# Kernel optimization log

Hardware: AMD Instinct MI355X
Metric: run time of the kernel (lower is better)

The kernel has to match this reference:

```python
import jax, jax.numpy as jnp
import numpy as np

N_NODES = 100000
N_EDGES = 600000
D_IN = 128
D_HID = 128
N_CLASSES = 64


def setup_inputs() -> dict:
    key = jax.random.key(0)
    ks = jax.random.split(key, 8)
    x = jax.random.normal(ks[0], (N_NODES, D_IN), dtype=jnp.float32)
    src = jax.random.randint(ks[1], (N_EDGES,), 0, N_NODES, dtype=jnp.int32)
    dst = jax.random.randint(ks[2], (N_EDGES,), 0, N_NODES, dtype=jnp.int32)
    s = 1.0 / np.sqrt(D_IN)
    W_self1 = jax.random.normal(ks[3], (D_IN, D_HID), dtype=jnp.float32) * s
    W_neigh1 = jax.random.normal(ks[4], (D_IN, D_HID), dtype=jnp.float32) * s
    b1 = jnp.zeros((D_HID,), dtype=jnp.float32)
    s2 = 1.0 / np.sqrt(D_HID)
    W_self2 = jax.random.normal(ks[5], (D_HID, N_CLASSES), dtype=jnp.float32) * s2
    W_neigh2 = jax.random.normal(ks[6], (D_HID, N_CLASSES), dtype=jnp.float32) * s2
    b2 = jnp.zeros((N_CLASSES,), dtype=jnp.float32)
    return {"x": x, "src": src, "dst": dst,
            "W_self1": W_self1, "W_neigh1": W_neigh1, "b1": b1,
            "W_self2": W_self2, "W_neigh2": W_neigh2, "b2": b2}


def _sage_conv(h, src, dst, W_self, W_neigh, b):
    # mean aggregation over in-neighbors (DGL SAGEConv 'mean')
    n = h.shape[0]
    nbr_sum = jax.ops.segment_sum(h[src], dst, num_segments=n)  # [N, d]
    deg = jax.ops.segment_sum(jnp.ones(src.shape, h.dtype), dst, num_segments=n)
    nbr_mean = nbr_sum / jnp.maximum(deg, 1.0)[:, None]
    return h @ W_self + nbr_mean @ W_neigh + b


def reference(x, src, dst, W_self1, W_neigh1, b1, W_self2, W_neigh2, b2):
    # dropout is identity in eval mode
    h = _sage_conv(x, src, dst, W_self1, W_neigh1, b1)
    h = jax.nn.relu(h)
    h = _sage_conv(h, src, dst, W_self2, W_neigh2, b2)
    return h
```

## Files before the change

kernel.cpp:

```cpp
#include <hip/hip_runtime.h>

#define N_NODES 100000
#define N_EDGES 600000
#define K_DIM 128
#define M2 64
#define NT_TILES ((N_NODES + 63) / 64)
#define GEMM_GRID 256

#define NBKT 800
#define NPB 125
#define HIST_BLOCKS 64
#define EPB (N_EDGES / HIST_BLOCKS)

using frag_ab = __attribute__((ext_vector_type(8))) short;
using frag_cd = __attribute__((ext_vector_type(4))) float;

__device__ __forceinline__ unsigned short f2b(float f) {
  unsigned u = __builtin_bit_cast(unsigned, f);
  u = (u + 0x7fffu + ((u >> 16) & 1u)) >> 16;
  return (unsigned short)u;
}

__device__ __forceinline__ void gload_lds16(const void* gsrc, void* ldst) {
  __builtin_amdgcn_global_load_lds(
      (const __attribute__((address_space(1))) void*)gsrc,
      (__attribute__((address_space(3))) void*)ldst, 16, 0, 0);
}

__device__ __forceinline__ void lgkm_barrier() {
  __builtin_amdgcn_sched_barrier(0);
  asm volatile("s_waitcnt lgkmcnt(0)" ::: "memory");
  __builtin_amdgcn_s_barrier();
  __builtin_amdgcn_sched_barrier(0);
}

#define XB_BLOCKS ((N_NODES * K_DIM / 4 + 255) / 256)
#define W_ELEMS ((128 + 128 + 64 + 64) * 128)
#define WB_BLOCKS ((W_ELEMS + 255) / 256)
__global__ __launch_bounds__(256) void conv_all(const float* __restrict__ x,
                                                unsigned short* __restrict__ xb,
                                                const float* __restrict__ Ws1,
                                                const float* __restrict__ Wn1,
                                                const float* __restrict__ Ws2,
                                                const float* __restrict__ Wn2,
                                                unsigned short* __restrict__ Ws1T,
                                                unsigned short* __restrict__ Wn1T,
                                                unsigned short* __restrict__ Ws2T,
                                                unsigned short* __restrict__ Wn2T,
                                                const int* __restrict__ dst,
                                                int* __restrict__ pos,
                                                int* __restrict__ gbucket,
                                                int* __restrict__ base_tbl) {
  __shared__ int lcnt[NBKT];
  if (blockIdx.x < HIST_BLOCKS) {
    int tid = threadIdx.x;
    for (int i = tid; i < NBKT; i += 256) lcnt[i] = 0;
    __syncthreads();
    int e0 = blockIdx.x * EPB;
    for (int e = e0 + tid; e < e0 + EPB; e += 256) {
      int b = dst[e] / NPB;
      pos[e] = atomicAdd(&lcnt[b], 1);
    }
    __syncthreads();
    for (int i = tid; i < NBKT; i += 256) {
      int c = lcnt[i];
      if (c) base_tbl[blockIdx.x * NBKT + i] = atomicAdd(&gbucket[i], c);
    }
  } else if (blockIdx.x < HIST_BLOCKS + XB_BLOCKS) {
    long i = (long)(blockIdx.x - HIST_BLOCKS) * 256 + threadIdx.x;
    if (i >= (long)N_NODES * K_DIM / 4) return;
    float4 v = *(const float4*)(x + i * 4);
    ushort4 o;
    o.x = f2b(v.x); o.y = f2b(v.y); o.z = f2b(v.z); o.w = f2b(v.w);
    *(ushort4*)(xb + i * 4) = o;
  } else {
    int i = (blockIdx.x - HIST_BLOCKS - XB_BLOCKS) * 256 + threadIdx.x;
    if (i >= W_ELEMS) return;
    const float* W;
    unsigned short* WT;
    int M, li;
    if (i < 128 * 128)               { W = Ws1; WT = Ws1T; M = 128; li = i; }
    else if (i < 2 * 128 * 128)      { W = Wn1; WT = Wn1T; M = 128; li = i - 128 * 128; }
    else if (i < 2 * 128 * 128 + 64 * 128) { W = Ws2; WT = Ws2T; M = 64; li = i - 2 * 128 * 128; }
    else                             { W = Wn2; WT = Wn2T; M = 64; li = i - 2 * 128 * 128 - 64 * 128; }
    int n = li >> 7, k = li & 127;
    WT[li] = f2b(W[k * M + n]);
  }
}

__global__ __launch_bounds__(1024) void scan_buckets(const int* __restrict__ gbucket,
                                                     int* __restrict__ bucket_start,
                                                     int* __restrict__ row_ptr) {
  __shared__ int s[1024];
  int tid = threadIdx.x;
  int v = (tid < NBKT) ? gbucket[tid] : 0;
  s[tid] = v;
  __syncthreads();
  for (int off = 1; off < 1024; off <<= 1) {
    int t = (tid >= off) ? s[tid - off] : 0;
    __syncthreads();
    s[tid] += t;
    __syncthreads();
  }
  if (tid < NBKT) bucket_start[tid] = s[tid] - v;
  if (tid == 0) { bucket_start[NBKT] = N_EDGES; row_ptr[N_NODES] = N_EDGES; }
}

__global__ __launch_bounds__(256) void bucket_scatter(const int* __restrict__ src,
                                                      const int* __restrict__ dst,
                                                      const int* __restrict__ pos,
                                                      const int* __restrict__ bucket_start,
                                                      const int* __restrict__ base_tbl,
                                                      int* __restrict__ ebuf_src,
                                                      int* __restrict__ ebuf_ln) {
  int e = blockIdx.x * 256 + threadIdx.x;
  if (e >= N_EDGES) return;
  int d = dst[e];
  int b = d / NPB;
  int p = bucket_start[b] + base_tbl[(e / EPB) * NBKT + b] + pos[e];
  ebuf_src[p] = src[e];
  ebuf_ln[p] = d - b * NPB;
}

__global__ __launch_bounds__(256) void bucket_csr(const int* __restrict__ ebuf_src,
                                                  const int* __restrict__ ebuf_ln,
                                                  const int* __restrict__ bucket_start,
                                                  int* __restrict__ row_ptr,
                                                  int* __restrict__ csr_src) {
  __shared__ int cnt[128];
  int tid = threadIdx.x, b = blockIdx.x;
  int bs = bucket_start[b], be = bucket_start[b + 1];
  for (int i = tid; i < 128; i += 256) cnt[i] = 0;
  __syncthreads();
  int ln[6], lp[6];
#pragma unroll
  for (int j = 0; j < 6; ++j) {
    int p = bs + tid + j * 256;
    if (p < be) { ln[j] = ebuf_ln[p]; lp[j] = atomicAdd(&cnt[ln[j]], 1); }
  }
  __syncthreads();
  for (int off = 1; off < 128; off <<= 1) {
    int t = 0;
    if (tid < 128 && tid >= off) t = cnt[tid - off];
    __syncthreads();
    if (tid < 128) cnt[tid] += t;
    __syncthreads();
  }
  for (int i = tid; i < NPB; i += 256)
    row_ptr[b * NPB + i] = bs + (i ? cnt[i - 1] : 0);
#pragma unroll
  for (int j = 0; j < 6; ++j) {
    int p = bs + tid + j * 256;
    if (p < be) {
      int l = ln[j];
      csr_src[bs + (l ? cnt[l - 1] : 0) + lp[j]] = ebuf_src[p];
    }
  }
}

__global__ __launch_bounds__(256) void aggregate128(const unsigned short* __restrict__ xb,
                                                    const int* __restrict__ row_ptr,
                                                    const int* __restrict__ csr_src,
                                                    unsigned short* __restrict__ agg, int n) {
  int t = blockIdx.x * blockDim.x + threadIdx.x;
  int node = t >> 4;
  int c = (t & 15) << 3;
  if (node >= n) return;
  int beg = row_ptr[node], end = row_ptr[node + 1];
  float acc[8];
#pragma unroll
  for (int j = 0; j < 8; ++j) acc[j] = 0.f;

  if (end > beg) {
    for (int e0 = beg; e0 < end; e0 += 8) {
      int idx[8];
#pragma unroll
      for (int p = 0; p < 8; ++p) idx[p] = csr_src[min(e0 + p, end - 1)];
      uint4 v[8];
#pragma unroll
      for (int p = 0; p < 8; ++p) v[p] = *(const uint4*)(xb + (size_t)idx[p] * K_DIM + c);
#pragma unroll
      for (int p = 0; p < 8; ++p) {
        float m = (e0 + p < end) ? 1.f : 0.f;
        unsigned u[4] = {v[p].x, v[p].y, v[p].z, v[p].w};
#pragma unroll
        for (int j = 0; j < 4; ++j) {
          acc[2 * j]     += m * __builtin_bit_cast(float, u[j] << 16);
          acc[2 * j + 1] += m * __builtin_bit_cast(float, u[j] & 0xffff0000u);
        }
      }
    }
  }
  float inv = 1.0f / (float)max(end - beg, 1);
  uint4 o;
  unsigned* op = (unsigned*)&o;
#pragma unroll
  for (int j = 0; j < 4; ++j) {
    unsigned lo = f2b(acc[2 * j] * inv);
    unsigned hi = f2b(acc[2 * j + 1] * inv);
    op[j] = lo | (hi << 16);
  }
  *(uint4*)(agg + (size_t)node * K_DIM + c) = o;
}

__global__ __launch_bounds__(256) void aggregate64_add(const unsigned short* __restrict__ g,
                                                       const int* __restrict__ row_ptr,
                                                       const int* __restrict__ csr_src,
                                                       float* __restrict__ out, int n) {
  int t = blockIdx.x * blockDim.x + threadIdx.x;
  int node = t >> 3;
  int c = (t & 7) << 3;
  if (node >= n) return;
  int beg = row_ptr[node], end = row_ptr[node + 1];
  float acc[8];
#pragma unroll
  for (int j = 0; j < 8; ++j) acc[j] = 0.f;

  if (end > beg) {
    for (int e0 = beg; e0 < end; e0 += 8) {
      int idx[8];
#pragma unroll
      for (int p = 0; p < 8; ++p) idx[p] = csr_src[min(e0 + p, end - 1)];
      uint4 v[8];
#pragma unroll
      for (int p = 0; p < 8; ++p) v[p] = *(const uint4*)(g + (size_t)idx[p] * M2 + c);
#pragma unroll
      for (int p = 0; p < 8; ++p) {
        float m = (e0 + p < end) ? 1.f : 0.f;
        unsigned u[4] = {v[p].x, v[p].y, v[p].z, v[p].w};
#pragma unroll
        for (int j = 0; j < 4; ++j) {
          acc[2 * j]     += m * __builtin_bit_cast(float, u[j] << 16);
          acc[2 * j + 1] += m * __builtin_bit_cast(float, u[j] & 0xffff0000u);
        }
      }
    }
  }
  float inv = 1.0f / (float)max(end - beg, 1);
  float* op = out + (size_t)node * M2 + c;
  float4 o0 = *(float4*)(op);
  float4 o1 = *(float4*)(op + 4);
  o0.x += acc[0] * inv; o0.y += acc[1] * inv; o0.z += acc[2] * inv; o0.w += acc[3] * inv;
  o1.x += acc[4] * inv; o1.y += acc[5] * inv; o1.z += acc[6] * inv; o1.w += acc[7] * inv;
  *(float4*)(op) = o0;
  *(float4*)(op + 4) = o1;
}

__device__ __forceinline__ void stage_tile(const unsigned short* xb, const unsigned short* aggb,
                                           int t, char* dstbase, int tid, int wave, int N) {
#pragma unroll
  for (int it = 0; it < 2; ++it) {
    int L = it * 8192 + tid * 16;
    int row = L >> 8;
    int srb = (L & 255) ^ ((row & 7) << 4);
    int node = t * 64 + row;
    if (node >= N) node = N - 1;
    char* d = dstbase + it * 8192 + wave * 1024;
    gload_lds16((const char*)xb + (size_t)node * 256 + srb, d);
    gload_lds16((const char*)aggb + (size_t)node * 256 + srb, d + 16384);
  }
}

__global__ __launch_bounds__(512, 2) void sage_fused_gemm(const unsigned short* __restrict__ xb,
                                                          const unsigned short* __restrict__ aggb,
                                                          const unsigned short* __restrict__ Ws1T,
                                                          const unsigned short* __restrict__ Wn1T,
                                                          const float* __restrict__ b1,
                                                          const unsigned short* __restrict__ Ws2T,
                                                          const unsigned short* __restrict__ Wn2T,
                                                          const float* __restrict__ b2,
                                                          float* __restrict__ out,
                                                          unsigned short* __restrict__ g, int N) {
  __shared__ char sL[163840];

  const int tid = threadIdx.x;
  const int wave = tid >> 6;
  const int lane = tid & 63;
  const int l15 = lane & 15;
  const int q = lane >> 4;
  const int nodeq = wave >> 1;
  const int fhalf = wave & 1;
  const int fbase = fhalf * 64;

#pragma unroll
  for (int it = 0; it < 4; ++it) {
    int L = it * 8192 + tid * 16;
    int row = L >> 8;
    int srb = (L & 255) ^ ((row & 7) << 4);
    char* d = sL + it * 8192 + wave * 1024;
    gload_lds16((const char*)Ws1T + row * 256 + srb, d);
    gload_lds16((const char*)Wn1T + row * 256 + srb, d + 32768);
  }
#pragma unroll
  for (int it = 0; it < 2; ++it) {
    int L = it * 8192 + tid * 16;
    int row = L >> 8;
    int srb = (L & 255) ^ ((row & 7) << 4);
    char* d = sL + 65536 + it * 8192 + wave * 1024;
    gload_lds16((const char*)Ws2T + row * 256 + srb, d);
    gload_lds16((const char*)Wn2T + row * 256 + srb, d + 16384);
  }
  int tt = blockIdx.x;
  if (tt < NT_TILES) stage_tile(xb, aggb, tt, sL + 98304, tid, wave, N);

  float4 bv1[4], bv2[4];
#pragma unroll
  for (int ft = 0; ft < 4; ++ft) {
    bv1[ft] = *(const float4*)(b1 + fbase + ft * 16 + q * 4);
    bv2[ft] = *(const float4*)(b2 + ft * 16 + q * 4);
  }

  int li = 0;
  for (; tt < NT_TILES; tt += GEMM_GRID, ++li) {
    char* cur = sL + 98304 + (li & 1) * 32768;
    char* nxt = sL + 98304 + ((li + 1) & 1) * 32768;

    __syncthreads();

    if (tt + GEMM_GRID < NT_TILES)
      stage_tile(xb, aggb, tt + GEMM_GRID, nxt, tid, wave, N);

    frag_cd acc[4];
#pragma unroll
    for (int ft = 0; ft < 4; ++ft) acc[ft] = (frag_cd)(0.f);

    const int xrow = nodeq * 16 + l15;
    const int xswz = (xrow & 7) << 4;
#pragma unroll
    for (int kb = 0; kb < 4; ++kb) {
      int base = kb * 64 + q * 16;
      frag_ab axk = *(const frag_ab*)(cur + xrow * 256 + (base ^ xswz));
      frag_ab agk = *(const frag_ab*)(cur + 16384 + xrow * 256 + (base ^ xswz));
      frag_ab fs[4], fn[4];
#pragma unroll
      for (int ft = 0; ft < 4; ++ft) {
        int wrow = fbase + ft * 16 + l15;
        int woff = base ^ ((wrow & 7) << 4);
        fs[ft] = *(const frag_ab*)(sL + wrow * 256 + woff);
        fn[ft] = *(const frag_ab*)(sL + 32768 + wrow * 256 + woff);
      }
#pragma unroll
      for (int ft = 0; ft < 4; ++ft) {
        acc[ft] = __builtin_amdgcn_mfma_f32_16x16x32_bf16(fs[ft], axk, acc[ft], 0, 0, 0);
        acc[ft] = __builtin_amdgcn_mfma_f32_16x16x32_bf16(fn[ft], agk, acc[ft], 0, 0, 0);
      }
    }

    lgkm_barrier();

#pragma unroll
    for (int ft = 0; ft < 4; ++ft) {
      int f0 = fbase + ft * 16 + q * 4;
      ushort4 o;
      o.x = f2b(fmaxf(acc[ft][0] + bv1[ft].x, 0.f));
      o.y = f2b(fmaxf(acc[ft][1] + bv1[ft].y, 0.f));
      o.z = f2b(fmaxf(acc[ft][2] + bv1[ft].z, 0.f));
      o.w = f2b(fmaxf(acc[ft][3] + bv1[ft].w, 0.f));
      *(ushort4*)(cur + xrow * 256 + ((f0 * 2) ^ xswz)) = o;
    }

    lgkm_barrier();

    const char* w2b = sL + 65536 + fhalf * 16384;
    frag_cd acc2[4];
#pragma unroll
    for (int ft = 0; ft < 4; ++ft) acc2[ft] = (frag_cd)(0.f);

#pragma unroll
    for (int kb = 0; kb < 4; ++kb) {
      int base = kb * 64 + q * 16;
      frag_ab ah = *(const frag_ab*)(cur + xrow * 256 + (base ^ xswz));
      frag_ab w2[4];
#pragma unroll
      for (int ft = 0; ft < 4; ++ft) {
        int wr = ft * 16 + l15;
        w2[ft] = *(const frag_ab*)(w2b + wr * 256 + (base ^ ((wr & 7) << 4)));
      }
#pragma unroll
      for (int ft = 0; ft < 4; ++ft)
        acc2[ft] = __builtin_amdgcn_mfma_f32_16x16x32_bf16(w2[ft], ah, acc2[ft], 0, 0, 0);
    }

    int node = tt * 64 + nodeq * 16 + l15;
    if (node < N) {
      if (fhalf == 0) {
#pragma unroll
        for (int ft = 0; ft < 4; ++ft) {
          int f0 = ft * 16 + q * 4;
          float4 o;
          o.x = acc2[ft][0] + bv2[ft].x;
          o.y = acc2[ft][1] + bv2[ft].y;
          o.z = acc2[ft][2] + bv2[ft].z;
          o.w = acc2[ft][3] + bv2[ft].w;
          *(float4*)(out + (size_t)node * M2 + f0) = o;
        }
      } else {
#pragma unroll
        for (int ft = 0; ft < 4; ++ft) {
          int f0 = ft * 16 + q * 4;
          ushort4 o;
          o.x = f2b(acc2[ft][0]);
          o.y = f2b(acc2[ft][1]);
          o.z = f2b(acc2[ft][2]);
          o.w = f2b(acc2[ft][3]);
          *(ushort4*)(g + (size_t)node * M2 + f0) = o;
        }
      }
    }
  }
}

extern "C" void kernel_launch(void* const* d_in, const int* in_sizes, int n_in,
                              void* d_out, int out_size, void* d_ws, size_t ws_size,
                              hipStream_t stream) {
  const float* x   = (const float*)d_in[0];
  const int*   src = (const int*)d_in[1];
  const int*   dst = (const int*)d_in[2];
  const float* Ws1 = (const float*)d_in[3];
  const float* Wn1 = (const float*)d_in[4];
  const float* b1  = (const float*)d_in[5];
  const float* Ws2 = (const float*)d_in[6];
  const float* Wn2 = (const float*)d_in[7];
  const float* b2  = (const float*)d_in[8];
  float* out = (float*)d_out;

  char* ws = (char*)d_ws;
  size_t off = 0;
  auto alloc = [&](size_t bytes) {
    void* p = ws + off;
    off = (off + bytes + 4095) & ~(size_t)4095;
    return p;
  };
  int* row_ptr      = (int*)alloc((size_t)(N_NODES + 1) * 4);
  int* pos          = (int*)alloc((size_t)N_EDGES * 4);
  int* gbucket      = (int*)alloc((size_t)NBKT * 4);
  int* bucket_start = (int*)alloc((size_t)(NBKT + 1) * 4);
  int* base_tbl     = (int*)alloc((size_t)HIST_BLOCKS * NBKT * 4);
  int* ebuf_src     = (int*)alloc((size_t)N_EDGES * 4);
  int* ebuf_ln      = (int*)alloc((size_t)N_EDGES * 4);
  int* csr_src      = (int*)alloc((size_t)N_EDGES * 4);
  unsigned short* xb   = (unsigned short*)alloc((size_t)N_NODES * K_DIM * 2);
  unsigned short* aggb = (unsigned short*)alloc((size_t)N_NODES * K_DIM * 2);
  unsigned short* g    = (unsigned short*)alloc((size_t)N_NODES * M2 * 2);
  unsigned short* Ws1T = (unsigned short*)alloc((size_t)128 * 128 * 2);
  unsigned short* Wn1T = (unsigned short*)alloc((size_t)128 * 128 * 2);
  unsigned short* Ws2T = (unsigned short*)alloc((size_t)64 * 128 * 2);
  unsigned short* Wn2T = (unsigned short*)alloc((size_t)64 * 128 * 2);

  hipMemsetAsync(gbucket, 0, (size_t)NBKT * 4, stream);

  conv_all<<<HIST_BLOCKS + XB_BLOCKS + WB_BLOCKS, 256, 0, stream>>>(
      x, xb, Ws1, Wn1, Ws2, Wn2, Ws1T, Wn1T, Ws2T, Wn2T, dst, pos, gbucket, base_tbl);

  scan_buckets<<<1, 1024, 0, stream>>>(gbucket, bucket_start, row_ptr);
  bucket_scatter<<<(N_EDGES + 255) / 256, 256, 0, stream>>>(
      src, dst, pos, bucket_start, base_tbl, ebuf_src, ebuf_ln);
  bucket_csr<<<NBKT, 256, 0, stream>>>(ebuf_src, ebuf_ln, bucket_start, row_ptr, csr_src);

  {
    long t = (long)N_NODES * 16;
    aggregate128<<<(int)((t + 255) / 256), 256, 0, stream>>>(xb, row_ptr, csr_src, aggb, N_NODES);
  }

  sage_fused_gemm<<<GEMM_GRID, 512, 0, stream>>>(
      xb, aggb, Ws1T, Wn1T, b1, Ws2T, Wn2T, b2, out, g, N_NODES);

  {
    long t = (long)N_NODES * 8;
    aggregate64_add<<<(int)((t + 255) / 256), 256, 0, stream>>>(g, row_ptr, csr_src, out, N_NODES);
  }
}
```

Before: 211.9 us.

## Fuse bucket CSR build with layer-1 neighbor aggregation in one kernel

Merges the per-bucket CSR construction and the layer-1 mean aggregation into one kernel with 512 threads per bucket. Sorted source indices are kept in shared memory and reused directly for the gather, so csr_src and row_ptr are not re-read from global memory. This also removes one kernel launch. The cost is that aggregation now runs on only 800 blocks, which may lower parallelism and latency hiding. Each thread handles at most 3 edges, so a bucket with more than 1536 edges would silently drop edges; the shared buffer has the same 1536 capacity.

```diff
diff --git a/kernel.cpp b/kernel.cpp
--- a/kernel.cpp
+++ b/kernel.cpp
@@ -11,6 +11,7 @@
 #define NPB 125
 #define HIST_BLOCKS 64
 #define EPB (N_EDGES / HIST_BLOCKS)
+#define BKT_CAP 1536
 
 using frag_ab = __attribute__((ext_vector_type(8))) short;
 using frag_cd = __attribute__((ext_vector_type(4))) float;
@@ -122,21 +123,29 @@
   ebuf_ln[p] = d - b * NPB;
 }
 
-__global__ __launch_bounds__(256) void bucket_csr(const int* __restrict__ ebuf_src,
-                                                  const int* __restrict__ ebuf_ln,
-                                                  const int* __restrict__ bucket_start,
-                                                  int* __restrict__ row_ptr,
-                                                  int* __restrict__ csr_src) {
+__global__ __launch_bounds__(512) void bucket_csr_agg1(const unsigned short* __restrict__ xb,
+                                                       const int* __restrict__ ebuf_src,
+                                                       const int* __restrict__ ebuf_ln,
+                                                       const int* __restrict__ bucket_start,
+                                                       int* __restrict__ row_ptr,
+                                                       int* __restrict__ csr_src,
+                                                       unsigned short* __restrict__ aggb) {
   __shared__ int cnt[128];
+  __shared__ int sedge[BKT_CAP];
   int tid = threadIdx.x, b = blockIdx.x;
   int bs = bucket_start[b], be = bucket_start[b + 1];
-  for (int i = tid; i < 128; i += 256) cnt[i] = 0;
+  for (int i = tid; i < 128; i += 512) cnt[i] = 0;
   __syncthreads();
-  int ln[6], lp[6];
-#pragma unroll
-  for (int j = 0; j < 6; ++j) {
-    int p = bs + tid + j * 256;
-    if (p < be) { ln[j] = ebuf_ln[p]; lp[j] = atomicAdd(&cnt[ln[j]], 1); }
+
+  int ln[3], lp[3], sv[3];
+#pragma unroll
+  for (int j = 0; j < 3; ++j) {
+    int p = bs + tid + j * 512;
+    if (p < be) {
+      ln[j] = ebuf_ln[p];
+      sv[j] = ebuf_src[p];
+      lp[j] = atomicAdd(&cnt[ln[j]], 1);
+    }
   }
   __syncthreads();
   for (int off = 1; off < 128; off <<= 1) {
@@ -146,61 +155,60 @@
     if (tid < 128) cnt[tid] += t;
     __syncthreads();
   }
-  for (int i = tid; i < NPB; i += 256)
+  for (int i = tid; i < NPB; i += 512)
     row_ptr[b * NPB + i] = bs + (i ? cnt[i - 1] : 0);
 #pragma unroll
-  for (int j = 0; j < 6; ++j) {
-    int p = bs + tid + j * 256;
+  for (int j = 0; j < 3; ++j) {
+    int p = bs + tid + j * 512;
     if (p < be) {
       int l = ln[j];
-      csr_src[bs + (l ? cnt[l - 1] : 0) + lp[j]] = ebuf_src[p];
-    }
-  }
-}
-
-__global__ __launch_bounds__(256) void aggregate128(const unsigned short* __restrict__ xb,
-                                                    const int* __restrict__ row_ptr,
-                                                    const int* __restrict__ csr_src,
-                                                    unsigned short* __restrict__ agg, int n) {
-  int t = blockIdx.x * blockDim.x + threadIdx.x;
-  int node = t >> 4;
-  int c = (t & 15) << 3;
-  if (node >= n) return;
-  int beg = row_ptr[node], end = row_ptr[node + 1];
-  float acc[8];
-#pragma unroll
-  for (int j = 0; j < 8; ++j) acc[j] = 0.f;
-
-  if (end > beg) {
-    for (int e0 = beg; e0 < end; e0 += 8) {
-      int idx[8];
-#pragma unroll
-      for (int p = 0; p < 8; ++p) idx[p] = csr_src[min(e0 + p, end - 1)];
-      uint4 v[8];
-#pragma unroll
-      for (int p = 0; p < 8; ++p) v[p] = *(const uint4*)(xb + (size_t)idx[p] * K_DIM + c);
-#pragma unroll
-      for (int p = 0; p < 8; ++p) {
-        float m = (e0 + p < end) ? 1.f : 0.f;
-        unsigned u[4] = {v[p].x, v[p].y, v[p].z, v[p].w};
-#pragma unroll
-        for (int j = 0; j < 4; ++j) {
-          acc[2 * j]     += m * __builtin_bit_cast(float, u[j] << 16);
-          acc[2 * j + 1] += m * __builtin_bit_cast(float, u[j] & 0xffff0000u);
+      int loc = (l ? cnt[l - 1] : 0) + lp[j];
+      sedge[loc] = sv[j];
+      csr_src[bs + loc] = sv[j];
+    }
+  }
+  __syncthreads();
+
+  int nl = tid >> 4;
+  int c = (tid & 15) << 3;
+  for (int n0 = 0; n0 < NPB; n0 += 32) {
+    int node = n0 + nl;
+    if (node < NPB) {
+      int beg = node ? cnt[node - 1] : 0;
+      int end = cnt[node];
+      float acc[8];
+#pragma unroll
+      for (int j = 0; j < 8; ++j) acc[j] = 0.f;
+      for (int e0 = beg; e0 < end; e0 += 8) {
+        int idx[8];
+#pragma unroll
+        for (int p = 0; p < 8; ++p) idx[p] = sedge[min(e0 + p, end - 1)];
+        uint4 v[8];
+#pragma unroll
+        for (int p = 0; p < 8; ++p) v[p] = *(const uint4*)(xb + (size_t)idx[p] * K_DIM + c);
+#pragma unroll
+        for (int p = 0; p < 8; ++p) {
+          float m = (e0 + p < end) ? 1.f : 0.f;
+          unsigned u[4] = {v[p].x, v[p].y, v[p].z, v[p].w};
+#pragma unroll
+          for (int j = 0; j < 4; ++j) {
+            acc[2 * j]     += m * __builtin_bit_cast(float, u[j] << 16);
+            acc[2 * j + 1] += m * __builtin_bit_cast(float, u[j] & 0xffff0000u);
+          }
         }
       }
-    }
-  }
-  float inv = 1.0f / (float)max(end - beg, 1);
-  uint4 o;
-  unsigned* op = (unsigned*)&o;
-#pragma unroll
-  for (int j = 0; j < 4; ++j) {
-    unsigned lo = f2b(acc[2 * j] * inv);
-    unsigned hi = f2b(acc[2 * j + 1] * inv);
-    op[j] = lo | (hi << 16);
-  }
-  *(uint4*)(agg + (size_t)node * K_DIM + c) = o;
+      float inv = 1.0f / (float)max(end - beg, 1);
+      uint4 o;
+      unsigned* op = (unsigned*)&o;
+#pragma unroll
+      for (int j = 0; j < 4; ++j) {
+        unsigned lo = f2b(acc[2 * j] * inv);
+        unsigned hi = f2b(acc[2 * j + 1] * inv);
+        op[j] = lo | (hi << 16);
+      }
+      *(uint4*)(aggb + (size_t)(b * NPB + node) * K_DIM + c) = o;
+    }
+  }
 }
 
 __global__ __launch_bounds__(256) void aggregate64_add(const unsigned short* __restrict__ g,
@@ -455,12 +463,9 @@
   scan_buckets<<<1, 1024, 0, stream>>>(gbucket, bucket_start, row_ptr);
   bucket_scatter<<<(N_EDGES + 255) / 256, 256, 0, stream>>>(
       src, dst, pos, bucket_start, base_tbl, ebuf_src, ebuf_ln);
-  bucket_csr<<<NBKT, 256, 0, stream>>>(ebuf_src, ebuf_ln, bucket_start, row_ptr, csr_src);
-
-  {
-    long t = (long)N_NODES * 16;
-    aggregate128<<<(int)((t + 255) / 256), 256, 0, stream>>>(xb, row_ptr, csr_src, aggb, N_NODES);
-  }
+
+  bucket_csr_agg1<<<NBKT, 512, 0, stream>>>(
+      xb, ebuf_src, ebuf_ln, bucket_start, row_ptr, csr_src, aggb);
 
   sage_fused_gemm<<<GEMM_GRID, 512, 0, stream>>>(
       xb, aggb, Ws1T, Wn1T, b1, Ws2T, Wn2T, b2, out, g, N_NODES);
```

Result: no change. 211.6 us (-0.1%).
